# Optimization experiments

Hardware: AMD Instinct MI355X
Metric: run time of the kernel (lower is better)

## Reference

```python
import jax, jax.numpy as jnp
import numpy as np

B, IC, OC, OUT_DIM, S = 64, 128, 128, 1024, 2
L = OUT_DIM * S  # 2048


def setup_inputs() -> dict:
    key = jax.random.key(0)
    k1, k2 = jax.random.split(key)
    x = jax.random.normal(k1, (B, IC, L), dtype=jnp.float32)
    weight = jax.random.normal(k2, (OC, IC, L), dtype=jnp.float32)
    return {"x": x, "weight": weight}


def reference(x, weight):
    # Faithful to: (x[:,None]*weight).view(B,OC,IC,-1,2).sum(dims=[-1,-3]) / sqrt(IC)
    # Fused as a single contraction over input_channels and the size-2 patch axis,
    # never materializing the (B,OC,IC,L) intermediate.
    ic = x.shape[1]
    xr = x.reshape(x.shape[0], ic, -1, 2)          # (B, IC, out_dim, 2)
    wr = weight.reshape(weight.shape[0], ic, -1, 2)  # (OC, IC, out_dim, 2)
    out = jnp.einsum('bids,oids->bod', xr, wr)       # (B, OC, out_dim)
    return out / jnp.sqrt(jnp.asarray(ic, dtype=x.dtype))
```

## Files before the change

kernel.cpp:

```cpp
#include <hip/hip_runtime.h>

#define B_SZ   64
#define IC_N   128
#define OC_N   128
#define OUT_D  1024
#define L_N    2048

typedef __attribute__((ext_vector_type(8))) __bf16          bf16x8;
typedef __attribute__((ext_vector_type(8))) unsigned short  u16x8;
typedef __attribute__((ext_vector_type(4))) float           f32x4;

__device__ __forceinline__ unsigned pack2bf(float lo, float hi) {
    unsigned ul = __builtin_bit_cast(unsigned, lo);
    unsigned uh = __builtin_bit_cast(unsigned, hi);
    ul += 0x7fffu + ((ul >> 16) & 1u);
    uh += 0x7fffu + ((uh >> 16) & 1u);
    return (ul >> 16) | (uh & 0xffff0000u);
}

__global__ __launch_bounds__(256, 4)
void repack_kernel(const float* __restrict__ x, const float* __restrict__ w,
                   unsigned short* __restrict__ xf, unsigned short* __restrict__ wf) {
    __shared__ unsigned tile2[32 * 260];

    const int bid = blockIdx.x;
    const int t    = threadIdx.x;
    const int ic_l = t & 15;
    const int r_l  = t >> 4;
    const int wv   = t >> 6, lane = t & 63;
    const int col  = lane & 15, quad = lane >> 4;

    const bool isw = (bid >= 256);
    int dg, ch, rg;
    if (!isw) { dg = bid & 7;  ch = (bid >> 3) & 7;  rg = bid >> 6; }
    else      { const int b2 = bid - 256; dg = b2 & 7; ch = (b2 >> 3) & 7; rg = b2 >> 6; }

    const float* src = isw ? w : x;
    const float* srow = src + (size_t)((rg * 16 + r_l) * 128 + ch * 16 + ic_l) * L_N + dg * 256;
    const int rowbase = ic_l + 16 * r_l;

    for (int p = 0; p < 4; ++p) {
        float4 v[16];
#pragma unroll
        for (int k = 0; k < 16; ++k)
            v[k] = *(const float4*)&srow[p * 64 + 4 * k];

        __syncthreads();

#pragma unroll
        for (int k = 0; k < 16; ++k) {
            tile2[(2 * k) * 260 + rowbase]     = pack2bf(v[k].x, v[k].y);
            tile2[(2 * k + 1) * 260 + rowbase] = pack2bf(v[k].z, v[k].w);
        }

        __syncthreads();

#pragma unroll
        for (int dd = 0; dd < 8; ++dd) {
            const int dl = wv * 8 + dd;
            const uint4 val = *(const uint4*)&tile2[dl * 260 + 16 * col + 4 * quad];
            const int d = dg * 128 + p * 32 + dl;
            size_t slot;
            unsigned short* dst;
            if (!isw) {
                slot = (((size_t)d * 8 + ch) * 4 + rg) * 64 + lane;
                dst = xf;
            } else {
                slot = ((((size_t)(rg >> 1) * 1024 + d) * 8 + ch) * 2 + (rg & 1)) * 64 + lane;
                dst = wf;
            }
            *(uint4*)&dst[slot * 8] = val;
        }
    }
}

__global__ __launch_bounds__(512, 2)
void gemm2_kernel(const unsigned short* __restrict__ xf,
                  const unsigned short* __restrict__ wf,
                  float* __restrict__ out) {
    __shared__ float eplds[16 * 64 * 10 + 8];

    const int bid = blockIdx.x;
    const int g   = (bid & 7) * 32 + (bid >> 3);
    const int och = g >> 7;
    const int dg  = g & 127;
    const int t = threadIdx.x, wv = t >> 6, lane = t & 63;
    const int col = lane & 15, quad = lane >> 4;
    const int d = dg * 8 + wv;

    const u16x8* xp = (const u16x8*)xf + (size_t)d * 2048 + lane;
    const u16x8* wp[4];
#pragma unroll
    for (int ntg = 0; ntg < 4; ++ntg) {
        const size_t ocb = och * 2 + (ntg >> 1);
        const size_t nt  = ntg & 1;
        wp[ntg] = (const u16x8*)wf + (((ocb * 1024 + d) * 8) * 2 + nt) * 64 + lane;
    }

    f32x4 acc[4][4];
#pragma unroll
    for (int mt = 0; mt < 4; ++mt)
#pragma unroll
        for (int ntg = 0; ntg < 4; ++ntg)
            acc[mt][ntg] = (f32x4){0.f, 0.f, 0.f, 0.f};

#pragma unroll
    for (int ch = 0; ch < 8; ++ch) {
        bf16x8 a[4], b[4];
#pragma unroll
        for (int mt = 0; mt < 4; ++mt)
            a[mt] = __builtin_bit_cast(bf16x8, xp[ch * 256 + mt * 64]);
#pragma unroll
        for (int ntg = 0; ntg < 4; ++ntg)
            b[ntg] = __builtin_bit_cast(bf16x8, wp[ntg][ch * 128]);
#pragma unroll
        for (int mt = 0; mt < 4; ++mt)
#pragma unroll
            for (int ntg = 0; ntg < 4; ++ntg)
                acc[mt][ntg] = __builtin_amdgcn_mfma_f32_16x16x32_bf16(
                    a[mt], b[ntg], acc[mt][ntg], 0, 0, 0);
    }

    const float scale = 0.088388347648318447f;
    const int o_base = och * 64;
#pragma unroll
    for (int r = 0; r < 4; ++r) {
        __syncthreads();
#pragma unroll
        for (int ntg = 0; ntg < 4; ++ntg)
#pragma unroll
            for (int reg = 0; reg < 4; ++reg)
                eplds[((4 * quad + reg) * 64 + ntg * 16 + col) * 10 + wv] =
                    acc[r][ntg][reg] * scale;
        __syncthreads();
#pragma unroll
        for (int pi = 0; pi < 2; ++pi) {
            const int P = t + pi * 512;
            const int b_l = P >> 6, o = P & 63;
            const float* s = &eplds[P * 10];
            float4 v0, v1;
            v0.x = s[0]; v0.y = s[1]; v0.z = s[2]; v0.w = s[3];
            v1.x = s[4]; v1.y = s[5]; v1.z = s[6]; v1.w = s[7];
            float* op = &out[(size_t)((16 * r + b_l) * 128 + o_base + o) * 1024 + dg * 8];
            *(float4*)op = v0;
            *(float4*)(op + 4) = v1;
        }
    }
}

#define D_TILE 8
#define N_TILE 32
#define KC     16
#define KPAD   40

__global__ __launch_bounds__(256, 2)
void lc1d_fallback(const float* __restrict__ x, const float* __restrict__ w,
                   float* __restrict__ out) {
    __shared__ __align__(16) unsigned short Xs[D_TILE][B_SZ][KPAD];
    __shared__ __align__(16) unsigned short Ws[D_TILE][N_TILE][KPAD];

    const int t     = threadIdx.x;
    const int wv_id = t >> 6;
    const int lane  = t & 63;
    const int col   = lane & 15;
    const int quad  = lane >> 4;

    const int oc_blk = blockIdx.x & 3;
    const int dg     = blockIdx.x >> 2;
    const int o0     = oc_blk * N_TILE;
    const int l0     = dg * (2 * D_TILE);

    f32x4 acc[2][4][2];
#pragma unroll
    for (int dl = 0; dl < 2; ++dl)
#pragma unroll
        for (int mt = 0; mt < 4; ++mt)
#pragma unroll
            for (int nt = 0; nt < 2; ++nt)
                acc[dl][mt][nt] = (f32x4){0.f, 0.f, 0.f, 0.f};

    for (int chunk = 0; chunk < IC_N / KC; ++chunk) {
        const int i0 = chunk * KC;
        float4 xv[16];
#pragma unroll
        for (int r = 0; r < 16; ++r) {
            const int f = t + 256 * r, b = f >> 6, il = (f >> 2) & 15, j = f & 3;
            xv[r] = *(const float4*)&x[(size_t)(b * IC_N + i0 + il) * L_N + l0 + 4 * j];
        }
        float4 wvv[8];
#pragma unroll
        for (int r = 0; r < 8; ++r) {
            const int f = t + 256 * r, ol = f >> 6, il = (f >> 2) & 15, j = f & 3;
            wvv[r] = *(const float4*)&w[(size_t)((o0 + ol) * IC_N + i0 + il) * L_N + l0 + 4 * j];
        }
        __syncthreads();
#pragma unroll
        for (int r = 0; r < 16; ++r) {
            const int f = t + 256 * r, b = f >> 6, il = (f >> 2) & 15, j = f & 3;
            *(unsigned*)&Xs[2 * j][b][2 * il]     = pack2bf(xv[r].x, xv[r].y);
            *(unsigned*)&Xs[2 * j + 1][b][2 * il] = pack2bf(xv[r].z, xv[r].w);
        }
#pragma unroll
        for (int r = 0; r < 8; ++r) {
            const int f = t + 256 * r, ol = f >> 6, il = (f >> 2) & 15, j = f & 3;
            *(unsigned*)&Ws[2 * j][ol][2 * il]     = pack2bf(wvv[r].x, wvv[r].y);
            *(unsigned*)&Ws[2 * j + 1][ol][2 * il] = pack2bf(wvv[r].z, wvv[r].w);
        }
        __syncthreads();
#pragma unroll
        for (int dl = 0; dl < 2; ++dl) {
            const int dp = 2 * wv_id + dl;
            bf16x8 afr[4];
            bf16x8 bfr[2];
#pragma unroll
            for (int mt = 0; mt < 4; ++mt)
                afr[mt] = __builtin_bit_cast(bf16x8, *(const u16x8*)&Xs[dp][16 * mt + col][quad * 8]);
#pragma unroll
            for (int nt = 0; nt < 2; ++nt)
                bfr[nt] = __builtin_bit_cast(bf16x8, *(const u16x8*)&Ws[dp][16 * nt + col][quad * 8]);
#pragma unroll
            for (int mt = 0; mt < 4; ++mt)
#pragma unroll
                for (int nt = 0; nt < 2; ++nt)
                    acc[dl][mt][nt] = __builtin_amdgcn_mfma_f32_16x16x32_bf16(
                        afr[mt], bfr[nt], acc[dl][mt][nt], 0, 0, 0);
        }
    }

    const float scale = 0.088388347648318447f;
    const int dbase = dg * D_TILE + 2 * wv_id;
#pragma unroll
    for (int mt = 0; mt < 4; ++mt)
#pragma unroll
        for (int nt = 0; nt < 2; ++nt)
#pragma unroll
            for (int reg = 0; reg < 4; ++reg) {
                const int b = 16 * mt + 4 * quad + reg;
                const int o = o0 + 16 * nt + col;
                float2 v2;
                v2.x = acc[0][mt][nt][reg] * scale;
                v2.y = acc[1][mt][nt][reg] * scale;
                *(float2*)&out[(size_t)(b * OC_N + o) * OUT_D + dbase] = v2;
            }
}

extern "C" void kernel_launch(void* const* d_in, const int* in_sizes, int n_in,
                              void* d_out, int out_size, void* d_ws, size_t ws_size,
                              hipStream_t stream) {
    const float* x = (const float*)d_in[0];
    const float* w = (const float*)d_in[1];
    float* out     = (float*)d_out;

    const size_t XF_BYTES = (size_t)B_SZ * IC_N * L_N * 2;
    const size_t WF_BYTES = (size_t)OC_N * IC_N * L_N * 2;

    if (ws_size >= XF_BYTES + WF_BYTES) {
        unsigned short* xf  = (unsigned short*)d_ws;
        unsigned short* wfp = (unsigned short*)((char*)d_ws + XF_BYTES);
        hipLaunchKernelGGL(repack_kernel, dim3(768), dim3(256), 0, stream, x, w, xf, wfp);
        hipLaunchKernelGGL(gemm2_kernel, dim3(256), dim3(512), 0, stream, xf, wfp, out);
    } else {
        hipLaunchKernelGGL(lc1d_fallback, dim3(512), dim3(256), 0, stream, x, w, out);
    }
}
```

Measured before the change: 300.0 us.

## Fuse bf16 repack into single GEMM kernel with register-prefetched LDS staging

Replaces the two-kernel path (a repack to a bf16 workspace, then an MFMA GEMM) and the fallback with one fused kernel. Each block loads fp32 x and weight slices for 4 output positions and all 128 output channels, converts them to bf16 in LDS, and prefetches the next input-channel chunk into registers while computing. This removes the workspace write and re-read and one launch, but the fp32 global loads are small strided float4 reads, and each block gets less work per fetched byte.

```diff
diff --git a/kernel.cpp b/kernel.cpp
--- a/kernel.cpp
+++ b/kernel.cpp
@@ -6,9 +6,8 @@
 #define OUT_D  1024
 #define L_N    2048
 
-typedef __attribute__((ext_vector_type(8))) __bf16          bf16x8;
-typedef __attribute__((ext_vector_type(8))) unsigned short  u16x8;
-typedef __attribute__((ext_vector_type(4))) float           f32x4;
+typedef __attribute__((ext_vector_type(8))) __bf16 bf16x8;
+typedef __attribute__((ext_vector_type(4))) float  f32x4;
 
 __device__ __forceinline__ unsigned pack2bf(float lo, float hi) {
     unsigned ul = __builtin_bit_cast(unsigned, lo);
@@ -18,230 +17,110 @@
     return (ul >> 16) | (uh & 0xffff0000u);
 }
 
-__global__ __launch_bounds__(256, 4)
-void repack_kernel(const float* __restrict__ x, const float* __restrict__ w,
-                   unsigned short* __restrict__ xf, unsigned short* __restrict__ wf) {
-    __shared__ unsigned tile2[32 * 260];
+__global__ __launch_bounds__(512)
+void lc1d_fused(const float* __restrict__ x, const float* __restrict__ w,
+                float* __restrict__ out) {
+    __shared__ __align__(16) unsigned smem[12288];
+    unsigned* Xs = smem;
+    unsigned* Ws = smem + 4096;
 
     const int bid = blockIdx.x;
-    const int t    = threadIdx.x;
-    const int ic_l = t & 15;
-    const int r_l  = t >> 4;
-    const int wv   = t >> 6, lane = t & 63;
-    const int col  = lane & 15, quad = lane >> 4;
-
-    const bool isw = (bid >= 256);
-    int dg, ch, rg;
-    if (!isw) { dg = bid & 7;  ch = (bid >> 3) & 7;  rg = bid >> 6; }
-    else      { const int b2 = bid - 256; dg = b2 & 7; ch = (b2 >> 3) & 7; rg = b2 >> 6; }
-
-    const float* src = isw ? w : x;
-    const float* srow = src + (size_t)((rg * 16 + r_l) * 128 + ch * 16 + ic_l) * L_N + dg * 256;
-    const int rowbase = ic_l + 16 * r_l;
-
-    for (int p = 0; p < 4; ++p) {
-        float4 v[16];
-#pragma unroll
-        for (int k = 0; k < 16; ++k)
-            v[k] = *(const float4*)&srow[p * 64 + 4 * k];
-
-        __syncthreads();
-
-#pragma unroll
-        for (int k = 0; k < 16; ++k) {
-            tile2[(2 * k) * 260 + rowbase]     = pack2bf(v[k].x, v[k].y);
-            tile2[(2 * k + 1) * 260 + rowbase] = pack2bf(v[k].z, v[k].w);
-        }
-
-        __syncthreads();
-
-#pragma unroll
-        for (int dd = 0; dd < 8; ++dd) {
-            const int dl = wv * 8 + dd;
-            const uint4 val = *(const uint4*)&tile2[dl * 260 + 16 * col + 4 * quad];
-            const int d = dg * 128 + p * 32 + dl;
-            size_t slot;
-            unsigned short* dst;
-            if (!isw) {
-                slot = (((size_t)d * 8 + ch) * 4 + rg) * 64 + lane;
-                dst = xf;
-            } else {
-                slot = ((((size_t)(rg >> 1) * 1024 + d) * 8 + ch) * 2 + (rg & 1)) * 64 + lane;
-                dst = wf;
-            }
-            *(uint4*)&dst[slot * 8] = val;
-        }
-    }
-}
-
-__global__ __launch_bounds__(512, 2)
-void gemm2_kernel(const unsigned short* __restrict__ xf,
-                  const unsigned short* __restrict__ wf,
-                  float* __restrict__ out) {
-    __shared__ float eplds[16 * 64 * 10 + 8];
-
-    const int bid = blockIdx.x;
-    const int g   = (bid & 7) * 32 + (bid >> 3);
-    const int och = g >> 7;
-    const int dg  = g & 127;
+    const int dg  = (bid & 7) * 32 + (bid >> 3);
     const int t = threadIdx.x, wv = t >> 6, lane = t & 63;
     const int col = lane & 15, quad = lane >> 4;
-    const int d = dg * 8 + wv;
 
-    const u16x8* xp = (const u16x8*)xf + (size_t)d * 2048 + lane;
-    const u16x8* wp[4];
-#pragma unroll
-    for (int ntg = 0; ntg < 4; ++ntg) {
-        const size_t ocb = och * 2 + (ntg >> 1);
-        const size_t nt  = ntg & 1;
-        wp[ntg] = (const u16x8*)wf + (((ocb * 1024 + d) * 8) * 2 + nt) * 64 + lane;
-    }
+    const int j   = t & 1;
+    const int icl = (t >> 1) & 15;
+    const int rb  = t >> 5;
+
+    const size_t rowoff  = ((size_t)rb * IC_N + icl) * L_N + (size_t)dg * 8 + 4 * j;
+    const float* xp = x + rowoff;
+    const float* wp = w + rowoff;
+    const size_t RSTRIDE = (size_t)16 * IC_N * L_N;
+    const size_t CSTRIDE = (size_t)16 * L_N;
+
+    const int dl = wv & 3, nh = wv >> 2;
+    const unsigned* xa = Xs + dl * 1024 + col * 16 + quad * 4;
+    const unsigned* wb = Ws + dl * 2048 + (nh * 64 + col) * 16 + quad * 4;
 
     f32x4 acc[4][4];
 #pragma unroll
     for (int mt = 0; mt < 4; ++mt)
 #pragma unroll
-        for (int ntg = 0; ntg < 4; ++ntg)
-            acc[mt][ntg] = (f32x4){0.f, 0.f, 0.f, 0.f};
+        for (int nt = 0; nt < 4; ++nt)
+            acc[mt][nt] = (f32x4){0.f, 0.f, 0.f, 0.f};
+
+    float4 xv[4], wvv[8];
+#pragma unroll
+    for (int r = 0; r < 4; ++r) xv[r]  = *(const float4*)(xp + (size_t)r * RSTRIDE);
+#pragma unroll
+    for (int r = 0; r < 8; ++r) wvv[r] = *(const float4*)(wp + (size_t)r * RSTRIDE);
+
+    for (int c = 0; c < 8; ++c) {
+        __syncthreads();
 
 #pragma unroll
-    for (int ch = 0; ch < 8; ++ch) {
-        bf16x8 a[4], b[4];
+        for (int r = 0; r < 4; ++r) {
+            const int b_ = rb + 16 * r;
+            Xs[(2 * j)     * 1024 + b_ * 16 + icl] = pack2bf(xv[r].x, xv[r].y);
+            Xs[(2 * j + 1) * 1024 + b_ * 16 + icl] = pack2bf(xv[r].z, xv[r].w);
+        }
+#pragma unroll
+        for (int r = 0; r < 8; ++r) {
+            const int o_ = rb + 16 * r;
+            Ws[(2 * j)     * 2048 + o_ * 16 + icl] = pack2bf(wvv[r].x, wvv[r].y);
+            Ws[(2 * j + 1) * 2048 + o_ * 16 + icl] = pack2bf(wvv[r].z, wvv[r].w);
+        }
+        __syncthreads();
+
+        if (c < 7) {
+            const float* xq = xp + (size_t)(c + 1) * CSTRIDE;
+            const float* wq = wp + (size_t)(c + 1) * CSTRIDE;
+#pragma unroll
+            for (int r = 0; r < 4; ++r) xv[r]  = *(const float4*)(xq + (size_t)r * RSTRIDE);
+#pragma unroll
+            for (int r = 0; r < 8; ++r) wvv[r] = *(const float4*)(wq + (size_t)r * RSTRIDE);
+        }
+
+        bf16x8 a[4], bfr[4];
 #pragma unroll
         for (int mt = 0; mt < 4; ++mt)
-            a[mt] = __builtin_bit_cast(bf16x8, xp[ch * 256 + mt * 64]);
+            a[mt] = __builtin_bit_cast(bf16x8, *(const uint4*)(xa + mt * 256));
 #pragma unroll
-        for (int ntg = 0; ntg < 4; ++ntg)
-            b[ntg] = __builtin_bit_cast(bf16x8, wp[ntg][ch * 128]);
+        for (int nt = 0; nt < 4; ++nt)
+            bfr[nt] = __builtin_bit_cast(bf16x8, *(const uint4*)(wb + nt * 256));
 #pragma unroll
         for (int mt = 0; mt < 4; ++mt)
 #pragma unroll
-            for (int ntg = 0; ntg < 4; ++ntg)
-                acc[mt][ntg] = __builtin_amdgcn_mfma_f32_16x16x32_bf16(
-                    a[mt], b[ntg], acc[mt][ntg], 0, 0, 0);
+            for (int nt = 0; nt < 4; ++nt)
+                acc[mt][nt] = __builtin_amdgcn_mfma_f32_16x16x32_bf16(
+                    a[mt], bfr[nt], acc[mt][nt], 0, 0, 0);
     }
 
     const float scale = 0.088388347648318447f;
-    const int o_base = och * 64;
+    float* ep = (float*)smem;
 #pragma unroll
     for (int r = 0; r < 4; ++r) {
         __syncthreads();
 #pragma unroll
-        for (int ntg = 0; ntg < 4; ++ntg)
+        for (int nt = 0; nt < 4; ++nt)
 #pragma unroll
-            for (int reg = 0; reg < 4; ++reg)
-                eplds[((4 * quad + reg) * 64 + ntg * 16 + col) * 10 + wv] =
-                    acc[r][ntg][reg] * scale;
+            for (int reg = 0; reg < 4; ++reg) {
+                const int b_l = 4 * quad + reg;
+                const int o   = nh * 64 + 16 * nt + col;
+                ep[(b_l * 128 + o) * 5 + dl] = acc[r][nt][reg] * scale;
+            }
         __syncthreads();
 #pragma unroll
-        for (int pi = 0; pi < 2; ++pi) {
-            const int P = t + pi * 512;
-            const int b_l = P >> 6, o = P & 63;
-            const float* s = &eplds[P * 10];
-            float4 v0, v1;
-            v0.x = s[0]; v0.y = s[1]; v0.z = s[2]; v0.w = s[3];
-            v1.x = s[4]; v1.y = s[5]; v1.z = s[6]; v1.w = s[7];
-            float* op = &out[(size_t)((16 * r + b_l) * 128 + o_base + o) * 1024 + dg * 8];
-            *(float4*)op = v0;
-            *(float4*)(op + 4) = v1;
+        for (int pi = 0; pi < 4; ++pi) {
+            const int P = t + 512 * pi;
+            const int b_l = P >> 7, o = P & 127;
+            const float* s = &ep[(size_t)P * 5];
+            float4 v;
+            v.x = s[0]; v.y = s[1]; v.z = s[2]; v.w = s[3];
+            *(float4*)&out[(size_t)((16 * r + b_l) * OC_N + o) * OUT_D + dg * 4] = v;
         }
     }
-}
-
-#define D_TILE 8
-#define N_TILE 32
-#define KC     16
-#define KPAD   40
-
-__global__ __launch_bounds__(256, 2)
-void lc1d_fallback(const float* __restrict__ x, const float* __restrict__ w,
-                   float* __restrict__ out) {
-    __shared__ __align__(16) unsigned short Xs[D_TILE][B_SZ][KPAD];
-    __shared__ __align__(16) unsigned short Ws[D_TILE][N_TILE][KPAD];
-
-    const int t     = threadIdx.x;
-    const int wv_id = t >> 6;
-    const int lane  = t & 63;
-    const int col   = lane & 15;
-    const int quad  = lane >> 4;
-
-    const int oc_blk = blockIdx.x & 3;
-    const int dg     = blockIdx.x >> 2;
-    const int o0     = oc_blk * N_TILE;
-    const int l0     = dg * (2 * D_TILE);
-
-    f32x4 acc[2][4][2];
-#pragma unroll
-    for (int dl = 0; dl < 2; ++dl)
-#pragma unroll
-        for (int mt = 0; mt < 4; ++mt)
-#pragma unroll
-            for (int nt = 0; nt < 2; ++nt)
-                acc[dl][mt][nt] = (f32x4){0.f, 0.f, 0.f, 0.f};
-
-    for (int chunk = 0; chunk < IC_N / KC; ++chunk) {
-        const int i0 = chunk * KC;
-        float4 xv[16];
-#pragma unroll
-        for (int r = 0; r < 16; ++r) {
-            const int f = t + 256 * r, b = f >> 6, il = (f >> 2) & 15, j = f & 3;
-            xv[r] = *(const float4*)&x[(size_t)(b * IC_N + i0 + il) * L_N + l0 + 4 * j];
-        }
-        float4 wvv[8];
-#pragma unroll
-        for (int r = 0; r < 8; ++r) {
-            const int f = t + 256 * r, ol = f >> 6, il = (f >> 2) & 15, j = f & 3;
-            wvv[r] = *(const float4*)&w[(size_t)((o0 + ol) * IC_N + i0 + il) * L_N + l0 + 4 * j];
-        }
-        __syncthreads();
-#pragma unroll
-        for (int r = 0; r < 16; ++r) {
-            const int f = t + 256 * r, b = f >> 6, il = (f >> 2) & 15, j = f & 3;
-            *(unsigned*)&Xs[2 * j][b][2 * il]     = pack2bf(xv[r].x, xv[r].y);
-            *(unsigned*)&Xs[2 * j + 1][b][2 * il] = pack2bf(xv[r].z, xv[r].w);
-        }
-#pragma unroll
-        for (int r = 0; r < 8; ++r) {
-            const int f = t + 256 * r, ol = f >> 6, il = (f >> 2) & 15, j = f & 3;
-            *(unsigned*)&Ws[2 * j][ol][2 * il]     = pack2bf(wvv[r].x, wvv[r].y);
-            *(unsigned*)&Ws[2 * j + 1][ol][2 * il] = pack2bf(wvv[r].z, wvv[r].w);
-        }
-        __syncthreads();
-#pragma unroll
-        for (int dl = 0; dl < 2; ++dl) {
-            const int dp = 2 * wv_id + dl;
-            bf16x8 afr[4];
-            bf16x8 bfr[2];
-#pragma unroll
-            for (int mt = 0; mt < 4; ++mt)
-                afr[mt] = __builtin_bit_cast(bf16x8, *(const u16x8*)&Xs[dp][16 * mt + col][quad * 8]);
-#pragma unroll
-            for (int nt = 0; nt < 2; ++nt)
-                bfr[nt] = __builtin_bit_cast(bf16x8, *(const u16x8*)&Ws[dp][16 * nt + col][quad * 8]);
-#pragma unroll
-            for (int mt = 0; mt < 4; ++mt)
-#pragma unroll
-                for (int nt = 0; nt < 2; ++nt)
-                    acc[dl][mt][nt] = __builtin_amdgcn_mfma_f32_16x16x32_bf16(
-                        afr[mt], bfr[nt], acc[dl][mt][nt], 0, 0, 0);
-        }
-    }
-
-    const float scale = 0.088388347648318447f;
-    const int dbase = dg * D_TILE + 2 * wv_id;
-#pragma unroll
-    for (int mt = 0; mt < 4; ++mt)
-#pragma unroll
-        for (int nt = 0; nt < 2; ++nt)
-#pragma unroll
-            for (int reg = 0; reg < 4; ++reg) {
-                const int b = 16 * mt + 4 * quad + reg;
-                const int o = o0 + 16 * nt + col;
-                float2 v2;
-                v2.x = acc[0][mt][nt][reg] * scale;
-                v2.y = acc[1][mt][nt][reg] * scale;
-                *(float2*)&out[(size_t)(b * OC_N + o) * OUT_D + dbase] = v2;
-            }
 }
 
 extern "C" void kernel_launch(void* const* d_in, const int* in_sizes, int n_in,
@@ -250,16 +129,5 @@
     const float* x = (const float*)d_in[0];
     const float* w = (const float*)d_in[1];
     float* out     = (float*)d_out;
-
-    const size_t XF_BYTES = (size_t)B_SZ * IC_N * L_N * 2;
-    const size_t WF_BYTES = (size_t)OC_N * IC_N * L_N * 2;
-
-    if (ws_size >= XF_BYTES + WF_BYTES) {
-        unsigned short* xf  = (unsigned short*)d_ws;
-        unsigned short* wfp = (unsigned short*)((char*)d_ws + XF_BYTES);
-        hipLaunchKernelGGL(repack_kernel, dim3(768), dim3(256), 0, stream, x, w, xf, wfp);
-        hipLaunchKernelGGL(gemm2_kernel, dim3(256), dim3(512), 0, stream, xf, wfp, out);
-    } else {
-        hipLaunchKernelGGL(lc1d_fallback, dim3(512), dim3(256), 0, stream, x, w, out);
-    }
+    hipLaunchKernelGGL(lc1d_fused, dim3(256), dim3(512), 0, stream, x, w, out);
 }
```

Result: faster. 289.0 us (-3.7%).
